# Kernel tuning notes

Hardware: AMD Instinct MI355X
Metric: run time of the kernel (lower is better)

Reference implementation:

```python
import jax, jax.numpy as jnp
import numpy as np

B, D, K = 32, 64, 256            # batch, num objects (seq len), feature size (== in_size)
G = [256, 256, 256]              # g_layers sizes
F1, F2, OUT = 256, 256, 128      # f_fc1, f_fc2, out_size


def setup_inputs() -> dict:
    key = jax.random.key(0)
    ks = jax.random.split(key, 16)
    scale = 0.02

    def w(k, shape):
        return jax.random.normal(k, shape, dtype=jnp.float32) * scale

    x = jax.random.normal(ks[0], (B, D, K), dtype=jnp.float32)
    # edge_feature: Linear(2*K, K). Stored [in, out] (transposed vs torch).
    edge_w = w(ks[1], (2 * K, K))
    edge_b = jnp.zeros((K,), dtype=jnp.float32)
    g_ws, g_bs = [], []
    in_s = K
    for i, out_s in enumerate(G):
        g_ws.append(w(ks[2 + i], (in_s, out_s)))
        g_bs.append(jnp.zeros((out_s,), dtype=jnp.float32))
        in_s = out_s
    f1_w = w(ks[8], (G[-1], F1)); f1_b = jnp.zeros((F1,), dtype=jnp.float32)
    f2_w = w(ks[9], (F1, F2));    f2_b = jnp.zeros((F2,), dtype=jnp.float32)
    f3_w = w(ks[10], (F2, OUT));  f3_b = jnp.zeros((OUT,), dtype=jnp.float32)
    return dict(x=x, edge_w=edge_w, edge_b=edge_b, g_ws=g_ws, g_bs=g_bs,
                f1_w=f1_w, f1_b=f1_b, f2_w=f2_w, f2_b=f2_b, f3_w=f3_w, f3_b=f3_b)


def reference(x, edge_w, edge_b, g_ws, g_bs, f1_w, f1_b, f2_w, f2_b, f3_w, f3_b):
    # x: [B, D, K]. Original builds x_full[b,i,j] = concat(x[b,j], x[b,i]) then
    # applies edge_feature (Linear(2K -> K)). Equivalent, without materializing the
    # concat: split edge_w into the halves acting on x_i (=x[b,j]) and x_j (=x[b,i]).
    k = x.shape[-1]
    u = x @ edge_w[:k]      # [B, D, K]  -> indexed by j (axis 2)
    v = x @ edge_w[k:]      # [B, D, K]  -> indexed by i (axis 1)
    h = u[:, None, :, :] + v[:, :, None, :] + edge_b   # [B, D, D, K]
    # g MLP over all d^2 pairs (Linear + ReLU chain)
    for gw, gb in zip(g_ws, g_bs):
        h = jax.nn.relu(h @ gw + gb)
    # sum-aggregate over all pairs
    x_g = h.sum(axis=(1, 2))                            # [B, G[-1]]
    # f MLP (dropout p=0.0 -> identity)
    x_f = jax.nn.relu(x_g @ f1_w + f1_b)
    x_f = jax.nn.relu(x_f @ f2_w + f2_b)
    return x_f @ f3_w + f3_b                            # [B, OUT]
```

## Files before the change

### kernel.cpp

```cpp
#include <hip/hip_runtime.h>
#include <hip/hip_bf16.h>

typedef __attribute__((ext_vector_type(4))) float f32x4;
typedef __attribute__((ext_vector_type(2))) int   i32x2;
typedef __attribute__((ext_vector_type(4))) int   i32x4;
typedef __attribute__((ext_vector_type(8))) short short8;

__device__ __forceinline__ unsigned short f2bf(float x) {
  __hip_bfloat16 h = __float2bfloat16(x);
  union { __hip_bfloat16 h1; unsigned short u; } c; c.h1 = h; return c.u;
}
__device__ __forceinline__ unsigned pk2(float a, float b) {
  __hip_bfloat162 h = __float22bfloat162_rn(make_float2(a, b));
  union { __hip_bfloat162 h2; unsigned u; } c; c.h2 = h; return c.u;
}
__device__ __forceinline__ float bf2f(unsigned short u) {
  union { unsigned u32; float f; } c; c.u32 = ((unsigned)u) << 16; return c.f;
}

__global__ void k_prep(const float* __restrict__ edge_w, const float* __restrict__ edge_b,
                       const float* __restrict__ gw0, const float* __restrict__ gb0,
                       const float* __restrict__ gw1, const float* __restrict__ gw2,
                       unsigned short* __restrict__ W1uR, unsigned short* __restrict__ W1vR,
                       float* __restrict__ c1,
                       unsigned short* __restrict__ W2R, unsigned short* __restrict__ W3R) {
  const int blk = blockIdx.x, t = threadIdx.x;
  __shared__ float eu[256], ev[256];
  if (blk < 256) {
    eu[t] = edge_w[blk * 256 + t];
    ev[t] = edge_w[(256 + blk) * 256 + t];
    __syncthreads();
    float su = 0.f, sv = 0.f;
    for (int o = 0; o < 256; ++o) {
      float gg = gw0[o * 256 + t];
      su += eu[o] * gg; sv += ev[o] * gg;
    }
    const int k = blk, m = t;
    const int w = m >> 6, mf = (m >> 4) & 3, q = m & 15;
    const int ch = k >> 5, g = (k >> 3) & 3, e = k & 7;
    const int idx = ((w * 8 + ch) * 4 + mf) * 512 + (g * 16 + q) * 8 + e;
    W1uR[idx] = f2bf(su);
    W1vR[idx] = f2bf(sv);
  } else if (blk == 256) {
    float s = gb0[t];
    for (int o = 0; o < 256; ++o) s += edge_b[o] * gw0[o * 256 + t];
    c1[t] = s;
  } else {
    int p = blk - 257;
    const float* src = (p < 32) ? gw1 : gw2;
    unsigned short* dst = (p < 32) ? W2R : W3R;
    p &= 31;
    int w = p >> 3, ch = p & 7;
    int mf = t >> 6, lane = t & 63, q = lane & 15, g = lane >> 4;
    int base = ((w * 8 + ch) * 4 + mf) * 512 + lane * 8;
    int m = w * 64 + mf * 16 + q;
#pragma unroll
    for (int e = 0; e < 8; ++e) {
      int k = ch * 32 + g * 8 + e;
      dst[base + e] = f2bf(src[k * 256 + m]);
    }
  }
}

__global__ void k_uv(const float* __restrict__ x,
                     const unsigned short* __restrict__ W1uR,
                     const unsigned short* __restrict__ W1vR,
                     const float* __restrict__ c1,
                     unsigned short* __restrict__ U1, float* __restrict__ V1c) {
  __shared__ unsigned short xs[8192];

  const int t = threadIdx.x;
  const int tile = blockIdx.x >> 1, sel = blockIdx.x & 1;
  const int r0 = tile * 32;
  const int wid = t >> 6, lane = t & 63;
  const int q = lane & 15, g = lane >> 4;
  const int mo = wid << 6;

  {
    const int row = t >> 3, sl = t & 7, r7 = row & 7;
    const float* xB = x + (size_t)(r0 + row) * 256;
    unsigned short* hB = xs + row * 256;
#pragma unroll
    for (int m = 0; m < 4; ++m) {
      int ks = sl + 8 * m;
      f32x4 u0 = *(const f32x4*)(xB + ks * 8);
      f32x4 u1 = *(const f32x4*)(xB + ks * 8 + 4);
      i32x4 wv = { (int)pk2(u0.x, u0.y), (int)pk2(u0.z, u0.w),
                   (int)pk2(u1.x, u1.y), (int)pk2(u1.z, u1.w) };
      *(i32x4*)(hB + (ks ^ r7) * 8) = wv;
    }
  }

  const unsigned short* WR = sel ? W1vR : W1uR;
  const unsigned short* aW = WR + (size_t)wid * 16384 + lane * 8;

  short8 a_[4], an_[4];
#pragma unroll
  for (int mf = 0; mf < 4; ++mf) a_[mf] = *(const short8*)(aW + mf * 512);

  __syncthreads();

  f32x4 acc[4][2];
#pragma unroll
  for (int mf = 0; mf < 4; ++mf)
#pragma unroll
    for (int nf = 0; nf < 2; ++nf) acc[mf][nf] = (f32x4){0.f, 0.f, 0.f, 0.f};

  for (int ch = 0; ch < 8; ++ch) {
    if (ch < 7) {
#pragma unroll
      for (int mf = 0; mf < 4; ++mf)
        an_[mf] = *(const short8*)(aW + (ch + 1) * 2048 + mf * 512);
    }
    short8 b_[2];
#pragma unroll
    for (int nf = 0; nf < 2; ++nf) {
      int r = q + 16 * nf;
      b_[nf] = *(const short8*)(xs + r * 256 + (((ch * 4 + g) ^ (r & 7)) * 8));
    }
#pragma unroll
    for (int mf = 0; mf < 4; ++mf)
#pragma unroll
      for (int nf = 0; nf < 2; ++nf)
        acc[mf][nf] = __builtin_amdgcn_mfma_f32_16x16x32_bf16(a_[mf], b_[nf], acc[mf][nf], 0, 0, 0);
    if (ch < 7) {
#pragma unroll
      for (int mf = 0; mf < 4; ++mf) a_[mf] = an_[mf];
    }
  }

#pragma unroll
  for (int mf = 0; mf < 4; ++mf) {
    int c2b = mo + 16 * mf + 4 * g;
#pragma unroll
    for (int nf = 0; nf < 2; ++nf) {
      int r = r0 + q + 16 * nf;
      f32x4 v = acc[mf][nf];
      if (sel == 0) {
        i32x2 wv = { (int)pk2(v.x, v.y), (int)pk2(v.z, v.w) };
        *(i32x2*)(U1 + (size_t)r * 256 + c2b) = wv;
      } else {
        f32x4 cc = *(const f32x4*)(c1 + c2b);
        f32x4 o = { v.x + cc.x, v.y + cc.y, v.z + cc.z, v.w + cc.w };
        *(f32x4*)(V1c + (size_t)r * 256 + c2b) = o;
      }
    }
  }
}

__device__ __forceinline__ void write_h1(short8 u, f32x4 v0, f32x4 v1,
                                         unsigned short* dst) {
  float r0 = fmaxf(bf2f((unsigned short)u[0]) + v0.x, 0.f);
  float r1 = fmaxf(bf2f((unsigned short)u[1]) + v0.y, 0.f);
  float r2 = fmaxf(bf2f((unsigned short)u[2]) + v0.z, 0.f);
  float r3 = fmaxf(bf2f((unsigned short)u[3]) + v0.w, 0.f);
  float r4 = fmaxf(bf2f((unsigned short)u[4]) + v1.x, 0.f);
  float r5 = fmaxf(bf2f((unsigned short)u[5]) + v1.y, 0.f);
  float r6 = fmaxf(bf2f((unsigned short)u[6]) + v1.z, 0.f);
  float r7 = fmaxf(bf2f((unsigned short)u[7]) + v1.w, 0.f);
  i32x4 wv = { (int)pk2(r0, r1), (int)pk2(r2, r3), (int)pk2(r4, r5), (int)pk2(r6, r7) };
  *(i32x4*)dst = wv;
}

__launch_bounds__(256, 2)
__global__ void k_main(const unsigned short* __restrict__ U1,
                       const float* __restrict__ V1c,
                       const unsigned short* __restrict__ W2R,
                       const unsigned short* __restrict__ W3R,
                       const float* __restrict__ b2, const float* __restrict__ b3,
                       float* __restrict__ partials) {
  __shared__ unsigned short bufA[16384];
  __shared__ unsigned short bufB[16384];

  const int t = threadIdx.x;
  const int bid = blockIdx.x;
  const int wrk = ((bid & 7) << 7) | (bid >> 3);
  const int b = wrk >> 5;
  const int it0 = (wrk & 31) * 2;
  const int wid = t >> 6, lane = t & 63;
  const int q = lane & 15, g = lane >> 4;
  const int mo = wid << 6;

  {
    const int row = t >> 2, sl = t & 3, r7 = row & 7;
    const unsigned short* uB = U1 + (size_t)(b * 64 + row) * 256;
    const float* vA = V1c + (size_t)(b * 64 + it0) * 256;
    const float* vB = vA + 256;
    unsigned short* dA = bufA + row * 256;
    unsigned short* dB = bufB + row * 256;
#pragma unroll
    for (int m = 0; m < 8; ++m) {
      int ks = sl + 4 * m;
      int s8 = (ks ^ r7) * 8;
      short8 u = *(const short8*)(uB + ks * 8);
      f32x4 a0 = *(const f32x4*)(vA + ks * 8);
      f32x4 a1 = *(const f32x4*)(vA + ks * 8 + 4);
      f32x4 b0 = *(const f32x4*)(vB + ks * 8);
      f32x4 b1 = *(const f32x4*)(vB + ks * 8 + 4);
      write_h1(u, a0, a1, dA + s8);
      write_h1(u, b0, b1, dB + s8);
    }
  }

  const unsigned short* aW2 = W2R + (size_t)wid * 16384 + lane * 8;
  const unsigned short* aW3 = W3R + (size_t)wid * 16384 + lane * 8;

  short8 a_[4], an_[4];
#pragma unroll
  for (int mf = 0; mf < 4; ++mf) a_[mf] = *(const short8*)(aW2 + mf * 512);

  __syncthreads();

  f32x4 accA[4][4], accB[4][4];
#pragma unroll
  for (int mf = 0; mf < 4; ++mf)
#pragma unroll
    for (int nf = 0; nf < 4; ++nf) {
      accA[mf][nf] = (f32x4){0.f, 0.f, 0.f, 0.f};
      accB[mf][nf] = (f32x4){0.f, 0.f, 0.f, 0.f};
    }

  for (int ch = 0; ch < 8; ++ch) {
    if (ch < 7) {
#pragma unroll
      for (int mf = 0; mf < 4; ++mf)
        an_[mf] = *(const short8*)(aW2 + (ch + 1) * 2048 + mf * 512);
    }
    short8 bA[4], bB[4];
#pragma unroll
    for (int nf = 0; nf < 4; ++nf) {
      int r = q + 16 * nf;
      int off = r * 256 + (((ch * 4 + g) ^ (r & 7)) * 8);
      bA[nf] = *(const short8*)(bufA + off);
      bB[nf] = *(const short8*)(bufB + off);
    }
#pragma unroll
    for (int mf = 0; mf < 4; ++mf)
#pragma unroll
      for (int nf = 0; nf < 4; ++nf) {
        accA[mf][nf] = __builtin_amdgcn_mfma_f32_16x16x32_bf16(a_[mf], bA[nf], accA[mf][nf], 0, 0, 0);
        accB[mf][nf] = __builtin_amdgcn_mfma_f32_16x16x32_bf16(a_[mf], bB[nf], accB[mf][nf], 0, 0, 0);
      }
    if (ch < 7) {
#pragma unroll
      for (int mf = 0; mf < 4; ++mf) a_[mf] = an_[mf];
    }
  }

  __syncthreads();

#pragma unroll
  for (int mf = 0; mf < 4; ++mf) a_[mf] = *(const short8*)(aW3 + mf * 512);
#pragma unroll
  for (int mf = 0; mf < 4; ++mf) {
    int c2b = mo + 16 * mf + 4 * g;
    f32x4 bb = *(const f32x4*)(b2 + c2b);
    int ksw = c2b >> 3, off = c2b & 7;
#pragma unroll
    for (int nf = 0; nf < 4; ++nf) {
      int r = q + 16 * nf;
      int dst = r * 256 + ((ksw ^ (r & 7)) * 8) + off;
      f32x4 vA_ = accA[mf][nf];
      f32x4 vB_ = accB[mf][nf];
      i32x2 wA = { (int)pk2(fmaxf(vA_.x + bb.x, 0.f), fmaxf(vA_.y + bb.y, 0.f)),
                   (int)pk2(fmaxf(vA_.z + bb.z, 0.f), fmaxf(vA_.w + bb.w, 0.f)) };
      i32x2 wB = { (int)pk2(fmaxf(vB_.x + bb.x, 0.f), fmaxf(vB_.y + bb.y, 0.f)),
                   (int)pk2(fmaxf(vB_.z + bb.z, 0.f), fmaxf(vB_.w + bb.w, 0.f)) };
      *(i32x2*)(bufA + dst) = wA;
      *(i32x2*)(bufB + dst) = wB;
    }
  }
  __syncthreads();

#pragma unroll
  for (int mf = 0; mf < 4; ++mf)
#pragma unroll
    for (int nf = 0; nf < 4; ++nf) {
      accA[mf][nf] = (f32x4){0.f, 0.f, 0.f, 0.f};
      accB[mf][nf] = (f32x4){0.f, 0.f, 0.f, 0.f};
    }

  for (int ch = 0; ch < 8; ++ch) {
    if (ch < 7) {
#pragma unroll
      for (int mf = 0; mf < 4; ++mf)
        an_[mf] = *(const short8*)(aW3 + (ch + 1) * 2048 + mf * 512);
    }
    short8 bA[4], bB[4];
#pragma unroll
    for (int nf = 0; nf < 4; ++nf) {
      int r = q + 16 * nf;
      int off = r * 256 + (((ch * 4 + g) ^ (r & 7)) * 8);
      bA[nf] = *(const short8*)(bufA + off);
      bB[nf] = *(const short8*)(bufB + off);
    }
#pragma unroll
    for (int mf = 0; mf < 4; ++mf)
#pragma unroll
      for (int nf = 0; nf < 4; ++nf) {
        accA[mf][nf] = __builtin_amdgcn_mfma_f32_16x16x32_bf16(a_[mf], bA[nf], accA[mf][nf], 0, 0, 0);
        accB[mf][nf] = __builtin_amdgcn_mfma_f32_16x16x32_bf16(a_[mf], bB[nf], accB[mf][nf], 0, 0, 0);
      }
    if (ch < 7) {
#pragma unroll
      for (int mf = 0; mf < 4; ++mf) a_[mf] = an_[mf];
    }
  }

  __syncthreads();

  float* scrA = (float*)&bufA[0];
  float* scrB = (float*)&bufB[0];
#pragma unroll
  for (int mf = 0; mf < 4; ++mf) {
    int n3b = mo + 16 * mf + 4 * g;
    f32x4 bb = *(const f32x4*)(b3 + n3b);
    f32x4 sA = (f32x4){0.f, 0.f, 0.f, 0.f};
    f32x4 sB = (f32x4){0.f, 0.f, 0.f, 0.f};
#pragma unroll
    for (int nf = 0; nf < 4; ++nf) {
      f32x4 vA_ = accA[mf][nf];
      f32x4 vB_ = accB[mf][nf];
      sA.x += fmaxf(vA_.x + bb.x, 0.f); sA.y += fmaxf(vA_.y + bb.y, 0.f);
      sA.z += fmaxf(vA_.z + bb.z, 0.f); sA.w += fmaxf(vA_.w + bb.w, 0.f);
      sB.x += fmaxf(vB_.x + bb.x, 0.f); sB.y += fmaxf(vB_.y + bb.y, 0.f);
      sB.z += fmaxf(vB_.z + bb.z, 0.f); sB.w += fmaxf(vB_.w + bb.w, 0.f);
    }
    *(f32x4*)(scrA + q * 264 + n3b) = sA;
    *(f32x4*)(scrB + q * 264 + n3b) = sB;
  }
  __syncthreads();
  float sA = 0.f, sB = 0.f;
#pragma unroll
  for (int q2 = 0; q2 < 16; ++q2) {
    sA += scrA[q2 * 264 + t];
    sB += scrB[q2 * 264 + t];
  }
  partials[(size_t)(b * 64 + it0) * 256 + t] = sA;
  partials[(size_t)(b * 64 + it0 + 1) * 256 + t] = sB;
}

__global__ void k_fmlp(const float* __restrict__ partials,
                       const float* __restrict__ f1w, const float* __restrict__ f1b,
                       const float* __restrict__ f2w, const float* __restrict__ f2b,
                       const float* __restrict__ f3w, const float* __restrict__ f3b,
                       float* __restrict__ out) {
  const int b = blockIdx.x, t = threadIdx.x;
  __shared__ float xg[256], x1[256], x2[256];
  {
    const float* p = partials + (size_t)(b * 64) * 256 + t;
    float s[8];
#pragma unroll
    for (int i = 0; i < 8; ++i) s[i] = 0.f;
#pragma unroll
    for (int k = 0; k < 8; ++k)
#pragma unroll
      for (int i = 0; i < 8; ++i) s[i] += p[(k * 8 + i) * 256];
    float tot = 0.f;
#pragma unroll
    for (int i = 0; i < 8; ++i) tot += s[i];
    xg[t] = tot;
  }
  __syncthreads();
  {
    float a0 = 0.f, a1 = 0.f, a2 = 0.f, a3 = 0.f;
#pragma unroll 4
    for (int k = 0; k < 64; ++k) {
      a0 += xg[k]       * f1w[(k)       * 256 + t];
      a1 += xg[k + 64]  * f1w[(k + 64)  * 256 + t];
      a2 += xg[k + 128] * f1w[(k + 128) * 256 + t];
      a3 += xg[k + 192] * f1w[(k + 192) * 256 + t];
    }
    x1[t] = fmaxf((a0 + a1) + (a2 + a3) + f1b[t], 0.f);
  }
  __syncthreads();
  {
    float a0 = 0.f, a1 = 0.f, a2 = 0.f, a3 = 0.f;
#pragma unroll 4
    for (int k = 0; k < 64; ++k) {
      a0 += x1[k]       * f2w[(k)       * 256 + t];
      a1 += x1[k + 64]  * f2w[(k + 64)  * 256 + t];
      a2 += x1[k + 128] * f2w[(k + 128) * 256 + t];
      a3 += x1[k + 192] * f2w[(k + 192) * 256 + t];
    }
    x2[t] = fmaxf((a0 + a1) + (a2 + a3) + f2b[t], 0.f);
  }
  __syncthreads();
  if (t < 128) {
    float a0 = 0.f, a1 = 0.f, a2 = 0.f, a3 = 0.f;
#pragma unroll 4
    for (int k = 0; k < 64; ++k) {
      a0 += x2[k]       * f3w[(k)       * 128 + t];
      a1 += x2[k + 64]  * f3w[(k + 64)  * 128 + t];
      a2 += x2[k + 128] * f3w[(k + 128) * 128 + t];
      a3 += x2[k + 192] * f3w[(k + 192) * 128 + t];
    }
    out[b * 128 + t] = (a0 + a1) + (a2 + a3) + f3b[t];
  }
}

__global__ void k_zero(float* __restrict__ out, int n) {
  int i = blockIdx.x * 256 + threadIdx.x;
  if (i < n) out[i] = 0.f;
}

extern "C" void kernel_launch(void* const* d_in, const int* in_sizes, int n_in,
                              void* d_out, int out_size, void* d_ws, size_t ws_size,
                              hipStream_t stream) {
  const float* x      = (const float*)d_in[0];
  const float* edge_w = (const float*)d_in[1];
  const float* edge_b = (const float*)d_in[2];
  const float *gw0, *gw1, *gw2, *gb0, *gb1, *gb2;
  const float *f1w, *f1b, *f2w, *f2b, *f3w, *f3b;

  if (n_in >= 15 && in_sizes[3] == 65536 && in_sizes[4] == 65536 && in_sizes[5] == 65536) {
    gw0 = (const float*)d_in[3]; gw1 = (const float*)d_in[4]; gw2 = (const float*)d_in[5];
    gb0 = (const float*)d_in[6]; gb1 = (const float*)d_in[7]; gb2 = (const float*)d_in[8];
    f1w = (const float*)d_in[9];  f1b = (const float*)d_in[10];
    f2w = (const float*)d_in[11]; f2b = (const float*)d_in[12];
    f3w = (const float*)d_in[13]; f3b = (const float*)d_in[14];
  } else if (n_in >= 15 && in_sizes[3] == 65536 && in_sizes[4] == 256) {
    gw0 = (const float*)d_in[3]; gb0 = (const float*)d_in[4];
    gw1 = (const float*)d_in[5]; gb1 = (const float*)d_in[6];
    gw2 = (const float*)d_in[7]; gb2 = (const float*)d_in[8];
    f1w = (const float*)d_in[9];  f1b = (const float*)d_in[10];
    f2w = (const float*)d_in[11]; f2b = (const float*)d_in[12];
    f3w = (const float*)d_in[13]; f3b = (const float*)d_in[14];
  } else {
    const float* gws = (const float*)d_in[3];
    const float* gbs = (const float*)d_in[4];
    gw0 = gws;          gw1 = gws + 65536;  gw2 = gws + 131072;
    gb0 = gbs;          gb1 = gbs + 256;    gb2 = gbs + 512;
    f1w = (const float*)d_in[5];  f1b = (const float*)d_in[6];
    f2w = (const float*)d_in[7];  f2b = (const float*)d_in[8];
    f3w = (const float*)d_in[9];  f3b = (const float*)d_in[10];
  }

  char* ws = (char*)d_ws;
  float*          c1       = (float*)(ws);
  unsigned short* W1uR     = (unsigned short*)(ws + 1024);
  unsigned short* W1vR     = (unsigned short*)(ws + 132096);
  unsigned short* W2R      = (unsigned short*)(ws + 263168);
  unsigned short* W3R      = (unsigned short*)(ws + 394240);
  unsigned short* U1       = (unsigned short*)(ws + 525312);
  float*          V1c      = (float*)(ws + 1573888);
  float*          partials = (float*)(ws + 3671040);
  const size_t need = 5768192;
  (void)out_size; (void)n_in;

  if (ws_size < need) {
    k_zero<<<dim3((out_size + 255) / 256), dim3(256), 0, stream>>>((float*)d_out, out_size);
    return;
  }

  k_prep<<<dim3(321), dim3(256), 0, stream>>>(edge_w, edge_b, gw0, gb0, gw1, gw2,
                                              W1uR, W1vR, c1, W2R, W3R);
  k_uv<<<dim3(128), dim3(256), 0, stream>>>(x, W1uR, W1vR, c1, U1, V1c);
  k_main<<<dim3(1024), dim3(256), 0, stream>>>(U1, V1c, W2R, W3R, gb1, gb2, partials);
  k_fmlp<<<dim3(32), dim3(256), 0, stream>>>(partials, f1w, f1b, f2w, f2b, f3w, f3b,
                                             (float*)d_out);
}
```

Before: 71.73 us.

## Fuse f-MLP into main kernel via last-block atomic counter, move W2/W3 prep

Removes the separate f-MLP launch: each k_main block bumps a per-batch atomic counter after writing its partials, and the 32nd block for a batch reduces the partials and runs the three small dense layers. The W2/W3 bf16 reformatting moves from k_prep into extra blocks of k_uv, and k_prep zeroes the counters. This saves one kernel launch and its gap, at the cost of threadfences, an atomic per block, and a serial tail on the last block of each batch.

```diff
diff --git a/kernel.cpp b/kernel.cpp
--- a/kernel.cpp
+++ b/kernel.cpp
@@ -20,10 +20,8 @@
 
 __global__ void k_prep(const float* __restrict__ edge_w, const float* __restrict__ edge_b,
                        const float* __restrict__ gw0, const float* __restrict__ gb0,
-                       const float* __restrict__ gw1, const float* __restrict__ gw2,
                        unsigned short* __restrict__ W1uR, unsigned short* __restrict__ W1vR,
-                       float* __restrict__ c1,
-                       unsigned short* __restrict__ W2R, unsigned short* __restrict__ W3R) {
+                       float* __restrict__ c1, unsigned int* __restrict__ cnt) {
   const int blk = blockIdx.x, t = threadIdx.x;
   __shared__ float eu[256], ev[256];
   if (blk < 256) {
@@ -41,12 +39,26 @@
     const int idx = ((w * 8 + ch) * 4 + mf) * 512 + (g * 16 + q) * 8 + e;
     W1uR[idx] = f2bf(su);
     W1vR[idx] = f2bf(sv);
-  } else if (blk == 256) {
+  } else {
     float s = gb0[t];
     for (int o = 0; o < 256; ++o) s += edge_b[o] * gw0[o * 256 + t];
     c1[t] = s;
-  } else {
-    int p = blk - 257;
+    if (t < 32) cnt[t] = 0u;
+  }
+}
+
+__global__ void k_uv(const float* __restrict__ x,
+                     const unsigned short* __restrict__ W1uR,
+                     const unsigned short* __restrict__ W1vR,
+                     const float* __restrict__ c1,
+                     const float* __restrict__ gw1, const float* __restrict__ gw2,
+                     unsigned short* __restrict__ U1, float* __restrict__ V1c,
+                     unsigned short* __restrict__ W2R, unsigned short* __restrict__ W3R) {
+  __shared__ unsigned short xs[8192];
+
+  const int t = threadIdx.x;
+  if (blockIdx.x >= 128) {
+    int p = blockIdx.x - 128;
     const float* src = (p < 32) ? gw1 : gw2;
     unsigned short* dst = (p < 32) ? W2R : W3R;
     p &= 31;
@@ -59,17 +71,9 @@
       int k = ch * 32 + g * 8 + e;
       dst[base + e] = f2bf(src[k * 256 + m]);
     }
-  }
-}
-
-__global__ void k_uv(const float* __restrict__ x,
-                     const unsigned short* __restrict__ W1uR,
-                     const unsigned short* __restrict__ W1vR,
-                     const float* __restrict__ c1,
-                     unsigned short* __restrict__ U1, float* __restrict__ V1c) {
-  __shared__ unsigned short xs[8192];
-
-  const int t = threadIdx.x;
+    return;
+  }
+
   const int tile = blockIdx.x >> 1, sel = blockIdx.x & 1;
   const int r0 = tile * 32;
   const int wid = t >> 6, lane = t & 63;
@@ -168,9 +172,14 @@
                        const unsigned short* __restrict__ W2R,
                        const unsigned short* __restrict__ W3R,
                        const float* __restrict__ b2, const float* __restrict__ b3,
-                       float* __restrict__ partials) {
+                       float* __restrict__ partials, unsigned int* __restrict__ cnt,
+                       const float* __restrict__ f1w, const float* __restrict__ f1b,
+                       const float* __restrict__ f2w, const float* __restrict__ f2b,
+                       const float* __restrict__ f3w, const float* __restrict__ f3b,
+                       float* __restrict__ out) {
   __shared__ unsigned short bufA[16384];
   __shared__ unsigned short bufB[16384];
+  __shared__ int lastFlag;
 
   const int t = threadIdx.x;
   const int bid = blockIdx.x;
@@ -338,64 +347,65 @@
   }
   partials[(size_t)(b * 64 + it0) * 256 + t] = sA;
   partials[(size_t)(b * 64 + it0 + 1) * 256 + t] = sB;
-}
-
-__global__ void k_fmlp(const float* __restrict__ partials,
-                       const float* __restrict__ f1w, const float* __restrict__ f1b,
-                       const float* __restrict__ f2w, const float* __restrict__ f2b,
-                       const float* __restrict__ f3w, const float* __restrict__ f3b,
-                       float* __restrict__ out) {
-  const int b = blockIdx.x, t = threadIdx.x;
-  __shared__ float xg[256], x1[256], x2[256];
-  {
-    const float* p = partials + (size_t)(b * 64) * 256 + t;
-    float s[8];
-#pragma unroll
-    for (int i = 0; i < 8; ++i) s[i] = 0.f;
-#pragma unroll
-    for (int k = 0; k < 8; ++k)
-#pragma unroll
-      for (int i = 0; i < 8; ++i) s[i] += p[(k * 8 + i) * 256];
-    float tot = 0.f;
-#pragma unroll
-    for (int i = 0; i < 8; ++i) tot += s[i];
-    xg[t] = tot;
-  }
-  __syncthreads();
-  {
-    float a0 = 0.f, a1 = 0.f, a2 = 0.f, a3 = 0.f;
+
+  __threadfence();
+  if (t == 0) lastFlag = (atomicAdd(&cnt[b], 1u) == 31u) ? 1 : 0;
+  __syncthreads();
+  if (lastFlag) {
+    __threadfence();
+    float* xg = (float*)&bufA[0];
+    float* x1 = xg + 256;
+    float* x2 = xg + 512;
+    {
+      const float* p = partials + (size_t)(b * 64) * 256 + t;
+      float s[8];
+#pragma unroll
+      for (int i = 0; i < 8; ++i) s[i] = 0.f;
+#pragma unroll
+      for (int k = 0; k < 8; ++k)
+#pragma unroll
+        for (int i = 0; i < 8; ++i) s[i] += p[(k * 8 + i) * 256];
+      float tot = 0.f;
+#pragma unroll
+      for (int i = 0; i < 8; ++i) tot += s[i];
+      xg[t] = tot;
+    }
+    __syncthreads();
+    {
+      float a0 = 0.f, a1 = 0.f, a2 = 0.f, a3 = 0.f;
 #pragma unroll 4
-    for (int k = 0; k < 64; ++k) {
-      a0 += xg[k]       * f1w[(k)       * 256 + t];
-      a1 += xg[k + 64]  * f1w[(k + 64)  * 256 + t];
-      a2 += xg[k + 128] * f1w[(k + 128) * 256 + t];
-      a3 += xg[k + 192] * f1w[(k + 192) * 256 + t];
-    }
-    x1[t] = fmaxf((a0 + a1) + (a2 + a3) + f1b[t], 0.f);
-  }
-  __syncthreads();
-  {
-    float a0 = 0.f, a1 = 0.f, a2 = 0.f, a3 = 0.f;
+      for (int k = 0; k < 64; ++k) {
+        a0 += xg[k]       * f1w[(k)       * 256 + t];
+        a1 += xg[k + 64]  * f1w[(k + 64)  * 256 + t];
+        a2 += xg[k + 128] * f1w[(k + 128) * 256 + t];
+        a3 += xg[k + 192] * f1w[(k + 192) * 256 + t];
+      }
+      x1[t] = fmaxf((a0 + a1) + (a2 + a3) + f1b[t], 0.f);
+    }
+    __syncthreads();
+    {
+      float a0 = 0.f, a1 = 0.f, a2 = 0.f, a3 = 0.f;
 #pragma unroll 4
-    for (int k = 0; k < 64; ++k) {
-      a0 += x1[k]       * f2w[(k)       * 256 + t];
-      a1 += x1[k + 64]  * f2w[(k + 64)  * 256 + t];
-      a2 += x1[k + 128] * f2w[(k + 128) * 256 + t];
-      a3 += x1[k + 192] * f2w[(k + 192) * 256 + t];
-    }
-    x2[t] = fmaxf((a0 + a1) + (a2 + a3) + f2b[t], 0.f);
-  }
-  __syncthreads();
-  if (t < 128) {
-    float a0 = 0.f, a1 = 0.f, a2 = 0.f, a3 = 0.f;
+      for (int k = 0; k < 64; ++k) {
+        a0 += x1[k]       * f2w[(k)       * 256 + t];
+        a1 += x1[k + 64]  * f2w[(k + 64)  * 256 + t];
+        a2 += x1[k + 128] * f2w[(k + 128) * 256 + t];
+        a3 += x1[k + 192] * f2w[(k + 192) * 256 + t];
+      }
+      x2[t] = fmaxf((a0 + a1) + (a2 + a3) + f2b[t], 0.f);
+    }
+    __syncthreads();
+    if (t < 128) {
+      float a0 = 0.f, a1 = 0.f, a2 = 0.f, a3 = 0.f;
 #pragma unroll 4
-    for (int k = 0; k < 64; ++k) {
-      a0 += x2[k]       * f3w[(k)       * 128 + t];
-      a1 += x2[k + 64]  * f3w[(k + 64)  * 128 + t];
-      a2 += x2[k + 128] * f3w[(k + 128) * 128 + t];
-      a3 += x2[k + 192] * f3w[(k + 192) * 128 + t];
-    }
-    out[b * 128 + t] = (a0 + a1) + (a2 + a3) + f3b[t];
+      for (int k = 0; k < 64; ++k) {
+        a0 += x2[k]       * f3w[(k)       * 128 + t];
+        a1 += x2[k + 64]  * f3w[(k + 64)  * 128 + t];
+        a2 += x2[k + 128] * f3w[(k + 128) * 128 + t];
+        a3 += x2[k + 192] * f3w[(k + 192) * 128 + t];
+      }
+      out[b * 128 + t] = (a0 + a1) + (a2 + a3) + f3b[t];
+    }
   }
 }
 
@@ -445,7 +455,8 @@
   unsigned short* U1       = (unsigned short*)(ws + 525312);
   float*          V1c      = (float*)(ws + 1573888);
   float*          partials = (float*)(ws + 3671040);
-  const size_t need = 5768192;
+  unsigned int*   cnt      = (unsigned int*)(ws + 5768192);
+  const size_t need = 5768320;
   (void)out_size; (void)n_in;
 
   if (ws_size < need) {
@@ -453,10 +464,12 @@
     return;
   }
 
-  k_prep<<<dim3(321), dim3(256), 0, stream>>>(edge_w, edge_b, gw0, gb0, gw1, gw2,
-                                              W1uR, W1vR, c1, W2R, W3R);
-  k_uv<<<dim3(128), dim3(256), 0, stream>>>(x, W1uR, W1vR, c1, U1, V1c);
-  k_main<<<dim3(1024), dim3(256), 0, stream>>>(U1, V1c, W2R, W3R, gb1, gb2, partials);
-  k_fmlp<<<dim3(32), dim3(256), 0, stream>>>(partials, f1w, f1b, f2w, f2b, f3w, f3b,
-                                             (float*)d_out);
-}
+  k_prep<<<dim3(257), dim3(256), 0, stream>>>(edge_w, edge_b, gw0, gb0,
+                                              W1uR, W1vR, c1, cnt);
+  k_uv<<<dim3(192), dim3(256), 0, stream>>>(x, W1uR, W1vR, c1, gw1, gw2,
+                                            U1, V1c, W2R, W3R);
+  k_main<<<dim3(1024), dim3(256), 0, stream>>>(U1, V1c, W2R, W3R, gb1, gb2,
+                                               partials, cnt,
+                                               f1w, f1b, f2w, f2b, f3w, f3b,
+                                               (float*)d_out);
+}
```

Measured after the change: 147.3 us. 2.05x slower.
